# Optimization experiments

Hardware: AMD Instinct MI355X
Metric: run time of the kernel (lower is better)

The kernel has to match this reference:

```python
import jax, jax.numpy as jnp
import numpy as np

GRID_MIN, GRID_MAX, NUM_GRIDS = -2.0, 2.0, 8
DENOM = (GRID_MAX - GRID_MIN) / (NUM_GRIDS - 1)
DIM, NUM_HEADS = 768, 12
B, N = 8, 1024


def _layer_norm(x, w, b, eps=1e-5):
    mu = jnp.mean(x, axis=-1, keepdims=True)
    var = jnp.mean((x - mu) ** 2, axis=-1, keepdims=True)
    return (x - mu) * jax.lax.rsqrt(var + eps) * w + b


def _fastkan(x, ln_w, ln_b, spline_w, base_w, base_b):
    # x: [..., C]; spline_w: [C*G, O]; base_w: [C, O]
    grid = jnp.linspace(GRID_MIN, GRID_MAX, NUM_GRIDS, dtype=x.dtype)
    h = _layer_norm(x, ln_w, ln_b)
    # RBF basis expansion: [..., C, G]
    basis = jnp.exp(-(((h[..., None] - grid) / DENOM) ** 2))
    basis = basis.reshape(*basis.shape[:-2], -1)  # [..., C*G]
    ret = basis @ spline_w
    ret = ret + jax.nn.silu(x) @ base_w + base_b
    return ret


def setup_inputs() -> dict:
    key = jax.random.key(0)
    ks = jax.random.split(key, 6)
    C = DIM
    return {
        "x": jax.random.normal(ks[0], (B, N, C), jnp.float32),
        "qkv_ln_w": jnp.ones((C,), jnp.float32),
        "qkv_ln_b": jnp.zeros((C,), jnp.float32),
        "qkv_spline_w": jax.random.normal(ks[1], (C * NUM_GRIDS, 3 * C), jnp.float32) * 0.1,
        "qkv_base_w": jax.random.normal(ks[2], (C, 3 * C), jnp.float32) * (1.0 / np.sqrt(C)),
        "qkv_base_b": jnp.zeros((3 * C,), jnp.float32),
        "proj_ln_w": jnp.ones((C,), jnp.float32),
        "proj_ln_b": jnp.zeros((C,), jnp.float32),
        "proj_spline_w": jax.random.normal(ks[3], (C * NUM_GRIDS, C), jnp.float32) * 0.1,
        "proj_base_w": jax.random.normal(ks[4], (C, C), jnp.float32) * (1.0 / np.sqrt(C)),
        "proj_base_b": jnp.zeros((C,), jnp.float32),
    }


def reference(x, qkv_ln_w, qkv_ln_b, qkv_spline_w, qkv_base_w, qkv_base_b,
              proj_ln_w, proj_ln_b, proj_spline_w, proj_base_w, proj_base_b):
    b, n, c = x.shape
    h = NUM_HEADS
    d = c // h
    scale = d ** -0.5
    qkv = _fastkan(x, qkv_ln_w, qkv_ln_b, qkv_spline_w, qkv_base_w, qkv_base_b)
    qkv = qkv.reshape(b, n, 3, h, d).transpose(2, 0, 3, 1, 4)  # [3,B,H,N,D]
    q, k, v = qkv[0], qkv[1], qkv[2]
    attn = jnp.einsum("bhnd,bhmd->bhnm", q, k) * scale
    attn = jax.nn.softmax(attn, axis=-1)
    out = jnp.einsum("bhnm,bhmd->bhnd", attn, v)
    out = out.transpose(0, 2, 1, 3).reshape(b, n, c)
    out = _fastkan(out, proj_ln_w, proj_ln_b, proj_spline_w, proj_base_w, proj_base_b)
    return out
```

## Files before the change

kernel.cpp:

```cpp
#include <hip/hip_runtime.h>
#include <cstdint>
#include <cstddef>

typedef _Float16 h8 __attribute__((ext_vector_type(8)));
typedef float f4 __attribute__((ext_vector_type(4)));

#define DEV static __device__ __forceinline__

DEV void gld16(const void* g, void* l) {
  __builtin_amdgcn_global_load_lds(
      (const __attribute__((address_space(1))) void*)g,
      (__attribute__((address_space(3))) void*)l, 16, 0, 0);
}

__global__ __launch_bounds__(256)
void kan_prep(const float* __restrict__ X, const float* __restrict__ lnw,
              const float* __restrict__ lnb, _Float16* __restrict__ Acat) {
  const int row = blockIdx.x;
  const int tid = threadIdx.x;
  const float* xr = X + (size_t)row * 768;
  float xv[3];
  xv[0] = xr[tid]; xv[1] = xr[tid + 256]; xv[2] = xr[tid + 512];
  float s = xv[0] + xv[1] + xv[2];
  float q = xv[0] * xv[0] + xv[1] * xv[1] + xv[2] * xv[2];
#pragma unroll
  for (int off = 32; off; off >>= 1) {
    s += __shfl_xor(s, off);
    q += __shfl_xor(q, off);
  }
  __shared__ float rs_[4], rq_[4];
  const int wave = tid >> 6;
  if ((tid & 63) == 0) { rs_[wave] = s; rq_[wave] = q; }
  __syncthreads();
  s = rs_[0] + rs_[1] + rs_[2] + rs_[3];
  q = rq_[0] + rq_[1] + rq_[2] + rq_[3];
  const float mu = s * (1.0f / 768.0f);
  const float var = q * (1.0f / 768.0f) - mu * mu;
  const float rsig = rsqrtf(var + 1e-5f);
  _Float16* out = Acat + (size_t)row * 6912;
#pragma unroll
  for (int i = 0; i < 3; ++i) {
    const int c = tid + i * 256;
    const float x = xv[i];
    const float h = (x - mu) * rsig * lnw[c] + lnb[c];
    union { h8 v; _Float16 u[8]; } bs;
#pragma unroll
    for (int g = 0; g < 8; ++g) {
      const float gv = -2.0f + (4.0f / 7.0f) * (float)g;
      const float t = (h - gv) * 1.75f;
      bs.u[g] = (_Float16)__expf(-t * t);
    }
    *(h8*)(out + c * 8) = bs.v;
    out[6144 + c] = (_Float16)(x / (1.0f + __expf(-x)));
  }
}

__global__ __launch_bounds__(256)
void wt_cast(const float* __restrict__ W, _Float16* __restrict__ Wt,
             int N, int koff) {
  __shared__ float t[32][33];
  const int k0 = blockIdx.x * 32, n0 = blockIdx.y * 32;
  const int tx = threadIdx.x & 31, ty = threadIdx.x >> 5;
#pragma unroll
  for (int i = 0; i < 4; ++i)
    t[ty + i * 8][tx] = W[(size_t)(k0 + ty + i * 8) * N + n0 + tx];
  __syncthreads();
#pragma unroll
  for (int i = 0; i < 4; ++i) {
    const int n = n0 + ty + i * 8;
    Wt[(size_t)n * 6912 + koff + k0 + tx] = (_Float16)t[tx][ty + i * 8];
  }
}

__global__ __launch_bounds__(256)
void v_transpose(const _Float16* __restrict__ qkv, _Float16* __restrict__ Vt) {
  const int bh = blockIdx.z, hh = bh % 12, b = bh / 12;
  const int kvb = blockIdx.x * 32, db = blockIdx.y * 32;
  __shared__ _Float16 t[32][33];
  const int tx = threadIdx.x & 31, ty = threadIdx.x >> 5;
#pragma unroll
  for (int i = 0; i < 4; ++i) {
    const int kv = kvb + ty + i * 8;
    t[ty + i * 8][tx] = qkv[(size_t)(b * 1024 + kv) * 2304 + 1536 + hh * 64 + db + tx];
  }
  __syncthreads();
#pragma unroll
  for (int i = 0; i < 4; ++i) {
    const int d = db + ty + i * 8;
    Vt[(size_t)(bh * 64 + d) * 1024 + kvb + tx] = t[tx][ty + i * 8];
  }
}

template <bool F16OUT>
__global__ __launch_bounds__(256)
void gemm_bt(const _Float16* __restrict__ A, const _Float16* __restrict__ Bt,
             const float* __restrict__ bias, void* __restrict__ Cout,
             int M, int N, int K) {
  __shared__ __align__(16) _Float16 As[128 * 64];
  __shared__ __align__(16) _Float16 Bs[128 * 64];
  const int tid = threadIdx.x;
  const int lane = tid & 63, wave = tid >> 6;
  const int bm = blockIdx.y * 128, bn = blockIdx.x * 128;
  const int rsub = lane >> 3;
  const int ksw = ((lane & 7) ^ rsub) * 8;
  const _Float16* ap[4];
  const _Float16* bp[4];
  _Float16* al[4];
  _Float16* bl[4];
#pragma unroll
  for (int i = 0; i < 4; ++i) {
    const int ch = wave * 4 + i;
    ap[i] = A + (size_t)(bm + ch * 8 + rsub) * K + ksw;
    bp[i] = Bt + (size_t)(bn + ch * 8 + rsub) * K + ksw;
    al[i] = As + ch * 512;
    bl[i] = Bs + ch * 512;
  }
  f4 acc[4][4] = {};
  const int wm = (wave >> 1) * 64, wn = (wave & 1) * 64;
  const int l16 = lane & 15, quad = lane >> 4, r7 = l16 & 7;
  const int nkt = K >> 6;
  for (int kt = 0; kt < nkt; ++kt) {
#pragma unroll
    for (int i = 0; i < 4; ++i) {
      gld16(ap[i], al[i]);
      gld16(bp[i], bl[i]);
      ap[i] += 64;
      bp[i] += 64;
    }
    __syncthreads();
    const h8* A8 = (const h8*)As;
    const h8* B8 = (const h8*)Bs;
#pragma unroll
    for (int ks = 0; ks < 2; ++ks) {
      const int kq = (ks * 4 + quad) ^ r7;
      h8 af[4], bfv[4];
#pragma unroll
      for (int mi = 0; mi < 4; ++mi) af[mi] = A8[(wm + mi * 16 + l16) * 8 + kq];
#pragma unroll
      for (int ni = 0; ni < 4; ++ni) bfv[ni] = B8[(wn + ni * 16 + l16) * 8 + kq];
#pragma unroll
      for (int mi = 0; mi < 4; ++mi)
#pragma unroll
        for (int ni = 0; ni < 4; ++ni)
          acc[mi][ni] = __builtin_amdgcn_mfma_f32_16x16x32_f16(af[mi], bfv[ni], acc[mi][ni], 0, 0, 0);
    }
    __syncthreads();
  }
#pragma unroll
  for (int ni = 0; ni < 4; ++ni) {
    const int col = bn + wn + ni * 16 + l16;
    const float bv = bias[col];
#pragma unroll
    for (int mi = 0; mi < 4; ++mi) {
#pragma unroll
      for (int j = 0; j < 4; ++j) {
        const int r = bm + wm + mi * 16 + quad * 4 + j;
        const float v = acc[mi][ni][j] + bv;
        if (F16OUT)
          ((_Float16*)Cout)[(size_t)r * N + col] = (_Float16)v;
        else
          ((float*)Cout)[(size_t)r * N + col] = v;
      }
    }
  }
}

__global__ __launch_bounds__(256)
void attn(const _Float16* __restrict__ qkv, const _Float16* __restrict__ Vt,
          float* __restrict__ ctx) {
  __shared__ __align__(16) _Float16 Qs[128 * 64];
  __shared__ __align__(16) _Float16 Ks[64 * 64];
  __shared__ __align__(16) _Float16 Vs[64 * 64];
  __shared__ __align__(16) _Float16 Ps[4 * 32 * 72];
  const int tid = threadIdx.x;
  const int lane = tid & 63, wave = tid >> 6;
  const int bh = blockIdx.y, hh = bh % 12, b = bh / 12;
  const int qt = blockIdx.x;
  const int rsub = lane >> 3;
  const int ksw = ((lane & 7) ^ rsub) * 8;
#pragma unroll
  for (int i = 0; i < 4; ++i) {
    const int ch = wave * 4 + i;
    const int row = ch * 8 + rsub;
    gld16(qkv + (size_t)(b * 1024 + qt * 128 + row) * 2304 + hh * 64 + ksw, Qs + ch * 512);
  }
  const int l16 = lane & 15, quad = lane >> 4, r7 = l16 & 7;
  f4 acc_o[2][4] = {};
  float m_old[2][4], l_sum[2][4];
#pragma unroll
  for (int mi = 0; mi < 2; ++mi)
#pragma unroll
    for (int j = 0; j < 4; ++j) { m_old[mi][j] = -1e30f; l_sum[mi][j] = 0.0f; }

  _Float16* Pw = Ps + wave * (32 * 72);

  for (int kv0 = 0; kv0 < 1024; kv0 += 64) {
#pragma unroll
    for (int i = 0; i < 2; ++i) {
      const int ch = wave * 2 + i;
      const int row = ch * 8 + rsub;
      gld16(qkv + (size_t)(b * 1024 + kv0 + row) * 2304 + 768 + hh * 64 + ksw, Ks + ch * 512);
      gld16(Vt + (size_t)(bh * 64 + row) * 1024 + kv0 + ksw, Vs + ch * 512);
    }
    __syncthreads();
    const h8* Q8 = (const h8*)Qs;
    const h8* K8 = (const h8*)Ks;
    const h8* V8 = (const h8*)Vs;
    f4 s[2][4] = {};
#pragma unroll
    for (int ks = 0; ks < 2; ++ks) {
      const int kq = (ks * 4 + quad) ^ r7;
      h8 qf[2], kf[4];
#pragma unroll
      for (int mi = 0; mi < 2; ++mi) qf[mi] = Q8[(wave * 32 + mi * 16 + l16) * 8 + kq];
#pragma unroll
      for (int ni = 0; ni < 4; ++ni) kf[ni] = K8[(ni * 16 + l16) * 8 + kq];
#pragma unroll
      for (int mi = 0; mi < 2; ++mi)
#pragma unroll
        for (int ni = 0; ni < 4; ++ni)
          s[mi][ni] = __builtin_amdgcn_mfma_f32_16x16x32_f16(qf[mi], kf[ni], s[mi][ni], 0, 0, 0);
    }
#pragma unroll
    for (int mi = 0; mi < 2; ++mi)
#pragma unroll
      for (int ni = 0; ni < 4; ++ni) s[mi][ni] *= 0.125f;
#pragma unroll
    for (int mi = 0; mi < 2; ++mi) {
#pragma unroll
      for (int j = 0; j < 4; ++j) {
        float vm = fmaxf(fmaxf(s[mi][0][j], s[mi][1][j]), fmaxf(s[mi][2][j], s[mi][3][j]));
#pragma unroll
        for (int off = 1; off < 16; off <<= 1) vm = fmaxf(vm, __shfl_xor(vm, off));
        const float mn = fmaxf(m_old[mi][j], vm);
        const float alpha = __expf(m_old[mi][j] - mn);
        float rs = 0.0f;
#pragma unroll
        for (int ni = 0; ni < 4; ++ni) {
          const float p = __expf(s[mi][ni][j] - mn);
          s[mi][ni][j] = p;
          rs += p;
        }
#pragma unroll
        for (int off = 1; off < 16; off <<= 1) rs += __shfl_xor(rs, off);
        l_sum[mi][j] = l_sum[mi][j] * alpha + rs;
        m_old[mi][j] = mn;
#pragma unroll
        for (int ni = 0; ni < 4; ++ni) acc_o[mi][ni][j] *= alpha;
      }
    }
#pragma unroll
    for (int mi = 0; mi < 2; ++mi)
#pragma unroll
      for (int ni = 0; ni < 4; ++ni)
#pragma unroll
        for (int j = 0; j < 4; ++j)
          Pw[(mi * 16 + quad * 4 + j) * 72 + ni * 16 + l16] = (_Float16)s[mi][ni][j];
#pragma unroll
    for (int ks = 0; ks < 2; ++ks) {
      const int kq = ks * 4 + quad;
      h8 pf[2], vf[4];
#pragma unroll
      for (int mi = 0; mi < 2; ++mi) pf[mi] = *(const h8*)(Pw + (mi * 16 + l16) * 72 + kq * 8);
#pragma unroll
      for (int ni = 0; ni < 4; ++ni) vf[ni] = V8[(ni * 16 + l16) * 8 + (kq ^ r7)];
#pragma unroll
      for (int mi = 0; mi < 2; ++mi)
#pragma unroll
        for (int ni = 0; ni < 4; ++ni)
          acc_o[mi][ni] = __builtin_amdgcn_mfma_f32_16x16x32_f16(pf[mi], vf[ni], acc_o[mi][ni], 0, 0, 0);
    }
    __syncthreads();
  }
#pragma unroll
  for (int mi = 0; mi < 2; ++mi) {
#pragma unroll
    for (int j = 0; j < 4; ++j) {
      const float inv = 1.0f / l_sum[mi][j];
      const int tok = b * 1024 + qt * 128 + wave * 32 + mi * 16 + quad * 4 + j;
      float* cr = ctx + (size_t)tok * 768 + hh * 64;
#pragma unroll
      for (int ni = 0; ni < 4; ++ni) cr[ni * 16 + l16] = acc_o[mi][ni][j] * inv;
    }
  }
}

extern "C" void kernel_launch(void* const* d_in, const int* in_sizes, int n_in,
                              void* d_out, int out_size, void* d_ws, size_t ws_size,
                              hipStream_t stream) {
  (void)in_sizes; (void)n_in; (void)out_size; (void)ws_size;
  const float* x    = (const float*)d_in[0];
  const float* qlnw = (const float*)d_in[1];
  const float* qlnb = (const float*)d_in[2];
  const float* qsw  = (const float*)d_in[3];
  const float* qbw  = (const float*)d_in[4];
  const float* qbb  = (const float*)d_in[5];
  const float* plnw = (const float*)d_in[6];
  const float* plnb = (const float*)d_in[7];
  const float* psw  = (const float*)d_in[8];
  const float* pbw  = (const float*)d_in[9];
  const float* pbb  = (const float*)d_in[10];
  float* out = (float*)d_out;

  _Float16* WtQ  = (_Float16*)d_ws;
  _Float16* WtP  = WtQ + (size_t)2304 * 6912;
  _Float16* Acat = WtP + (size_t)768 * 6912;
  _Float16* QKV  = Acat + (size_t)8192 * 6912;
  _Float16* Vt   = QKV + (size_t)8192 * 2304;
  float* CTX = (float*)(Vt + (size_t)96 * 64 * 1024);

  dim3 blk(256);
  wt_cast<<<dim3(192, 72), blk, 0, stream>>>(qsw, WtQ, 2304, 0);
  wt_cast<<<dim3(24, 72),  blk, 0, stream>>>(qbw, WtQ, 2304, 6144);
  wt_cast<<<dim3(192, 24), blk, 0, stream>>>(psw, WtP, 768, 0);
  wt_cast<<<dim3(24, 24),  blk, 0, stream>>>(pbw, WtP, 768, 6144);
  kan_prep<<<8192, blk, 0, stream>>>(x, qlnw, qlnb, Acat);
  gemm_bt<true><<<dim3(2304 / 128, 8192 / 128), blk, 0, stream>>>(
      Acat, WtQ, qbb, QKV, 8192, 2304, 6912);
  v_transpose<<<dim3(32, 2, 96), blk, 0, stream>>>(QKV, Vt);
  attn<<<dim3(8, 96), blk, 0, stream>>>(QKV, Vt, CTX);
  kan_prep<<<8192, blk, 0, stream>>>(CTX, plnw, plnb, Acat);
  gemm_bt<false><<<dim3(768 / 128, 8192 / 128), blk, 0, stream>>>(
      Acat, WtP, pbb, out, 8192, 768, 6912);
}
```

Baseline: 807.2 us.

## Switch GEMM to 32x32x16 MFMA and split-K the projection GEMM

The GEMM inner loop now uses 32x32x16 f16 MFMA instructions with a 2x2 accumulator tile per wave instead of 16x16x32 with 4x4, which halves the number of LDS fragment loads per MFMA. The projection GEMM, which only launches 384 blocks, is split along K into two slices writing fp32 partials into the reused QKV buffer. A new ksum2 kernel adds the two partials plus the bias. This is meant to fill more compute units, at the cost of extra partial-sum traffic and one more launch.

New measurement: 747.9 us. 7.3% less time.

```diff
diff --git a/kernel.cpp b/kernel.cpp
--- a/kernel.cpp
+++ b/kernel.cpp
@@ -4,6 +4,7 @@
 
 typedef _Float16 h8 __attribute__((ext_vector_type(8)));
 typedef float f4 __attribute__((ext_vector_type(4)));
+typedef float f16f __attribute__((ext_vector_type(16)));
 
 #define DEV static __device__ __forceinline__
 
@@ -95,12 +96,14 @@
 __global__ __launch_bounds__(256)
 void gemm_bt(const _Float16* __restrict__ A, const _Float16* __restrict__ Bt,
              const float* __restrict__ bias, void* __restrict__ Cout,
-             int M, int N, int K) {
+             int N, int ldK, int kLen, size_t sliceStride) {
   __shared__ __align__(16) _Float16 As[128 * 64];
   __shared__ __align__(16) _Float16 Bs[128 * 64];
   const int tid = threadIdx.x;
   const int lane = tid & 63, wave = tid >> 6;
   const int bm = blockIdx.y * 128, bn = blockIdx.x * 128;
+  const int slice = blockIdx.z;
+  const int kOff = slice * kLen;
   const int rsub = lane >> 3;
   const int ksw = ((lane & 7) ^ rsub) * 8;
   const _Float16* ap[4];
@@ -110,15 +113,15 @@
 #pragma unroll
   for (int i = 0; i < 4; ++i) {
     const int ch = wave * 4 + i;
-    ap[i] = A + (size_t)(bm + ch * 8 + rsub) * K + ksw;
-    bp[i] = Bt + (size_t)(bn + ch * 8 + rsub) * K + ksw;
+    ap[i] = A + (size_t)(bm + ch * 8 + rsub) * ldK + kOff + ksw;
+    bp[i] = Bt + (size_t)(bn + ch * 8 + rsub) * ldK + kOff + ksw;
     al[i] = As + ch * 512;
     bl[i] = Bs + ch * 512;
   }
-  f4 acc[4][4] = {};
+  f16f acc[2][2] = {};
   const int wm = (wave >> 1) * 64, wn = (wave & 1) * 64;
-  const int l16 = lane & 15, quad = lane >> 4, r7 = l16 & 7;
-  const int nkt = K >> 6;
+  const int l31 = lane & 31, half = lane >> 5, r7 = lane & 7;
+  const int nkt = kLen >> 6;
   for (int kt = 0; kt < nkt; ++kt) {
 #pragma unroll
     for (int i = 0; i < 4; ++i) {
@@ -131,38 +134,50 @@
     const h8* A8 = (const h8*)As;
     const h8* B8 = (const h8*)Bs;
 #pragma unroll
-    for (int ks = 0; ks < 2; ++ks) {
-      const int kq = (ks * 4 + quad) ^ r7;
-      h8 af[4], bfv[4];
-#pragma unroll
-      for (int mi = 0; mi < 4; ++mi) af[mi] = A8[(wm + mi * 16 + l16) * 8 + kq];
-#pragma unroll
-      for (int ni = 0; ni < 4; ++ni) bfv[ni] = B8[(wn + ni * 16 + l16) * 8 + kq];
-#pragma unroll
-      for (int mi = 0; mi < 4; ++mi)
-#pragma unroll
-        for (int ni = 0; ni < 4; ++ni)
-          acc[mi][ni] = __builtin_amdgcn_mfma_f32_16x16x32_f16(af[mi], bfv[ni], acc[mi][ni], 0, 0, 0);
+    for (int ks = 0; ks < 4; ++ks) {
+      const int o = (ks * 2 + half) ^ r7;
+      h8 af[2], bfv[2];
+#pragma unroll
+      for (int mi = 0; mi < 2; ++mi) af[mi] = A8[(wm + mi * 32 + l31) * 8 + o];
+#pragma unroll
+      for (int ni = 0; ni < 2; ++ni) bfv[ni] = B8[(wn + ni * 32 + l31) * 8 + o];
+#pragma unroll
+      for (int mi = 0; mi < 2; ++mi)
+#pragma unroll
+        for (int ni = 0; ni < 2; ++ni)
+          acc[mi][ni] = __builtin_amdgcn_mfma_f32_32x32x16_f16(af[mi], bfv[ni], acc[mi][ni], 0, 0, 0);
     }
     __syncthreads();
   }
 #pragma unroll
-  for (int ni = 0; ni < 4; ++ni) {
-    const int col = bn + wn + ni * 16 + l16;
-    const float bv = bias[col];
-#pragma unroll
-    for (int mi = 0; mi < 4; ++mi) {
-#pragma unroll
-      for (int j = 0; j < 4; ++j) {
-        const int r = bm + wm + mi * 16 + quad * 4 + j;
-        const float v = acc[mi][ni][j] + bv;
+  for (int ni = 0; ni < 2; ++ni) {
+    const int col = bn + wn + ni * 32 + l31;
+    const float bv = F16OUT ? bias[col] : 0.0f;
+#pragma unroll
+    for (int mi = 0; mi < 2; ++mi) {
+      const int rb = bm + wm + mi * 32 + 4 * half;
+#pragma unroll
+      for (int reg = 0; reg < 16; ++reg) {
+        const int r = rb + (reg & 3) + 8 * (reg >> 2);
+        const float v = acc[mi][ni][reg] + bv;
         if (F16OUT)
           ((_Float16*)Cout)[(size_t)r * N + col] = (_Float16)v;
         else
-          ((float*)Cout)[(size_t)r * N + col] = v;
+          ((float*)Cout + slice * sliceStride)[(size_t)r * N + col] = v;
       }
     }
   }
+}
+
+__global__ __launch_bounds__(256)
+void ksum2(const float* __restrict__ P, const float* __restrict__ bias,
+           float* __restrict__ out) {
+  const size_t off = ((size_t)blockIdx.x * 256 + threadIdx.x) * 4;
+  const int col = (int)(off % 768);
+  f4 a = *(const f4*)(P + off);
+  f4 b = *(const f4*)(P + (size_t)8192 * 768 + off);
+  f4 c = *(const f4*)(bias + col);
+  *(f4*)(out + off) = a + b + c;
 }
 
 __global__ __launch_bounds__(256)
@@ -308,6 +323,7 @@
   _Float16* QKV  = Acat + (size_t)8192 * 6912;
   _Float16* Vt   = QKV + (size_t)8192 * 2304;
   float* CTX = (float*)(Vt + (size_t)96 * 64 * 1024);
+  float* Pp = (float*)QKV;
 
   dim3 blk(256);
   wt_cast<<<dim3(192, 72), blk, 0, stream>>>(qsw, WtQ, 2304, 0);
@@ -315,11 +331,12 @@
   wt_cast<<<dim3(192, 24), blk, 0, stream>>>(psw, WtP, 768, 0);
   wt_cast<<<dim3(24, 24),  blk, 0, stream>>>(pbw, WtP, 768, 6144);
   kan_prep<<<8192, blk, 0, stream>>>(x, qlnw, qlnb, Acat);
-  gemm_bt<true><<<dim3(2304 / 128, 8192 / 128), blk, 0, stream>>>(
-      Acat, WtQ, qbb, QKV, 8192, 2304, 6912);
+  gemm_bt<true><<<dim3(2304 / 128, 8192 / 128, 1), blk, 0, stream>>>(
+      Acat, WtQ, qbb, QKV, 2304, 6912, 6912, 0);
   v_transpose<<<dim3(32, 2, 96), blk, 0, stream>>>(QKV, Vt);
   attn<<<dim3(8, 96), blk, 0, stream>>>(QKV, Vt, CTX);
   kan_prep<<<8192, blk, 0, stream>>>(CTX, plnw, plnb, Acat);
-  gemm_bt<false><<<dim3(768 / 128, 8192 / 128), blk, 0, stream>>>(
-      Acat, WtP, pbb, out, 8192, 768, 6912);
-}
+  gemm_bt<false><<<dim3(768 / 128, 8192 / 128, 2), blk, 0, stream>>>(
+      Acat, WtP, nullptr, Pp, 768, 6912, 3456, (size_t)8192 * 768);
+  ksum2<<<8192 * 768 / 4 / 256, blk, 0, stream>>>(Pp, pbb, out);
+}
```
